# Optimization experiments

Hardware: AMD Instinct MI355X
Metric: run time of the kernel (lower is better)

## Reference

```python
import jax, jax.numpy as jnp
import numpy as np

B, IN, H, OUT, RANK = 2048, 256, 128, 128, 8
EPS = 1e-5

def setup_inputs() -> dict:
    key = jax.random.key(0)
    ks = jax.random.split(key, 9)
    inv = lambda n: 1.0 / np.sqrt(n)
    return {
        "X": jax.random.normal(ks[0], (B, IN), jnp.float32),
        "W1": jax.random.uniform(ks[1], (IN, H), jnp.float32, -inv(IN), inv(IN)),
        "b1": jnp.zeros((H,), jnp.float32),
        "W2": jax.random.uniform(ks[2], (IN, OUT), jnp.float32, -inv(IN), inv(IN)),
        "b2": jnp.zeros((OUT,), jnp.float32),
        "W3": jax.random.uniform(ks[3], (H, OUT), jnp.float32, -inv(H), inv(H)),
        "b3": jnp.zeros((OUT,), jnp.float32),
        "P": jax.random.normal(ks[4], (RANK, H, H, H), jnp.float32),  # (rank, p, q, k)
        "gz": jnp.ones((H,), jnp.float32),
        "bz": jnp.zeros((H,), jnp.float32),
        "gy": jnp.ones((H,), jnp.float32),
        "by": jnp.zeros((H,), jnp.float32),
    }

def _bn(x, g, b):
    # training-mode BatchNorm1d: batch stats, biased variance
    m = x.mean(axis=0)
    v = x.var(axis=0)
    return (x - m) * jax.lax.rsqrt(v + EPS) * g + b

def reference(X, W1, b1, W2, b2, W3, b3, P, gz, bz, gy, by):
    Z = jax.nn.relu(X @ W1 + b1)               # (B, H); dropout = identity (eval)

    def step(carry, Pi):
        Zi, Y = carry
        # batch_quadratic: out[b,k] = sum_{p,q} Zi[b,p] * Pi[p,q,k] * Z[b,q]
        Zi = jnp.einsum('bp,pqk,bq->bk', Zi, Pi, Z)
        Zi = _bn(Zi, gz, bz)
        return (Zi, Y + Zi / RANK), None

    Y0 = jnp.zeros((X.shape[0], H), X.dtype)
    (_, Y), _ = jax.lax.scan(step, (Z, Y0), P)
    Y = _bn(Y, gy, by)
    out = jax.nn.relu(jax.nn.relu(Y @ W3 + b3) + jax.nn.relu(X @ W2 + b2))
    return out
```

## Files before the change

### kernel.cpp

```cpp
#include <hip/hip_runtime.h>

typedef __bf16 bf16x8 __attribute__((ext_vector_type(8)));
typedef float  floatx4 __attribute__((ext_vector_type(4)));

constexpr int B_    = 2048;
constexpr int NIN   = 256;
constexpr int H_    = 128;
constexpr int RANK_ = 8;
constexpr float EPS_ = 1e-5f;

__global__ __launch_bounds__(256)
void k_head(const float* __restrict__ X,
            const float* __restrict__ W1, const float* __restrict__ b1,
            const float* __restrict__ W2, const float* __restrict__ b2,
            const float* __restrict__ P,
            float* __restrict__ Z, float* __restrict__ R2, __bf16* __restrict__ Zbf,
            __bf16* __restrict__ Pperm, float* __restrict__ stats ) {
    __shared__ float sT[32 * 129];
    const int bx = blockIdx.x, t = threadIdx.x;

    if (bx < RANK_ + 1) stats[bx * 256 + t] = 0.f;

    {
        const int row0 = bx * 2;
        sT[t]       = X[(size_t)row0       * NIN + t];
        sT[256 + t] = X[(size_t)(row0 + 1) * NIN + t];
        __syncthreads();
        const int col = t & 127, half = t >> 7;
        float s1 = 0.f, s2 = 0.f;
        const float* sxh = sT + half * 256;
#pragma unroll 8
        for (int i = 0; i < NIN; ++i) {
            s1 = fmaf(sxh[i], W1[i * H_ + col], s1);
            s2 = fmaf(sxh[i], W2[i * H_ + col], s2);
        }
        const int b = row0 + half;
        const float z = fmaxf(s1 + b1[col], 0.f);
        const float r = fmaxf(s2 + b2[col], 0.f);
        Z[(size_t)b * H_ + col]   = z;
        Zbf[(size_t)b * H_ + col] = (__bf16)z;
        R2[(size_t)b * H_ + col]  = r;
        __syncthreads();
    }
    {
        const int r = bx >> 7, p = bx & 127;
        const float4* Pp4 = (const float4*)(P + ((size_t)r * H_ + p) * (H_ * H_));
        __bf16* dst = Pperm + (size_t)r * (H_ * H_ * H_);
        const int L = t & 63, quad = L >> 4, lo = L & 15, g0 = t >> 6;
#pragma unroll
        for (int s = 0; s < 4; ++s) {
#pragma unroll
            for (int it = 0; it < 4; ++it) {
                const int idx = it * 256 + t;
                const int q = idx >> 5, k4 = idx & 31;
                const float4 v = Pp4[(size_t)(s * 32 + q) * 32 + k4];
                float* d = sT + q * 129 + k4 * 4;
                d[0] = v.x; d[1] = v.y; d[2] = v.z; d[3] = v.w;
            }
            __syncthreads();
#pragma unroll
            for (int gg = 0; gg < 2; ++gg) {
                const int g = g0 + 4 * gg;
                __bf16 v8[8];
#pragma unroll
                for (int j = 0; j < 8; ++j)
                    v8[j] = (__bf16)sT[(quad * 8 + j) * 129 + g * 16 + lo];
                *(bf16x8*)(dst + (((size_t)(g * 128 + p) * 4 + s) * 64 + L) * 8) =
                    *(const bf16x8*)v8;
            }
            __syncthreads();
        }
    }
}

__global__ __launch_bounds__(512, 2)
void k_rank(const __bf16* __restrict__ Pr, const __bf16* __restrict__ Zbf,
            const float* __restrict__ prevT, const float* __restrict__ prevStats,
            const float* __restrict__ gz, const float* __restrict__ bz,
            float* __restrict__ T, float* __restrict__ stats, const int first) {
    __shared__ float smem[8960];
    const int kg = blockIdx.x, mblk = blockIdx.y, b0 = mblk * 64;
    const int t = threadIdx.x;
    const int w = t >> 6, L = t & 63, quad = L >> 4, lo = L & 15;

    float* sAl = smem + 8704; float* sBe = smem + 8832;
    if (t < 128) {
        if (first) { sAl[t] = 1.f; sBe[t] = 0.f; }
        else {
            const float s1 = prevStats[t], s2 = prevStats[128 + t];
            const float mm = s1 * (1.f / B_);
            const float var = s2 * (1.f / B_) - mm * mm;
            const float a = rsqrtf(var + EPS_) * gz[t];
            sAl[t] = a; sBe[t] = bz[t] - mm * a;
        }
    }
    bf16x8 A[4][4];
#pragma unroll
    for (int mt = 0; mt < 4; ++mt)
#pragma unroll
        for (int ks = 0; ks < 4; ++ks)
            A[mt][ks] = *(const bf16x8*)(Zbf + (size_t)(b0 + mt * 16 + lo) * H_ + ks * 32 + quad * 8);
    __syncthreads();
    {
        const int sp = t & 127, rr = t >> 7;
        const float a = sAl[sp], be = sBe[sp];
#pragma unroll
        for (int i = 0; i < 16; ++i) {
            const int row = rr + 4 * i;
            smem[sp * 68 + row] = fmaf(prevT[(size_t)(b0 + row) * H_ + sp], a, be);
        }
    }
    __syncthreads();

    floatx4 acc[4];
#pragma unroll
    for (int mt = 0; mt < 4; ++mt) acc[mt] = (floatx4){0.f, 0.f, 0.f, 0.f};

    const bf16x8* Pb = (const bf16x8*)Pr;
    const int p0 = w * 16;
    const size_t fbase = ((size_t)kg * 128 + p0) * 4;
    bf16x8 Bf[4], Bn[4];
#pragma unroll
    for (int s = 0; s < 4; ++s) Bf[s] = Pb[(fbase + s) * 64 + L];

    for (int pp = 0; pp < 16; ++pp) {
        const int p = p0 + pp;
        if (pp < 15) {
#pragma unroll
            for (int s = 0; s < 4; ++s)
                Bn[s] = Pb[(fbase + (size_t)(pp + 1) * 4 + s) * 64 + L];
        }
        floatx4 S[4];
#pragma unroll
        for (int mt = 0; mt < 4; ++mt) S[mt] = (floatx4){0.f, 0.f, 0.f, 0.f};
#pragma unroll
        for (int ks = 0; ks < 4; ++ks)
#pragma unroll
            for (int mt = 0; mt < 4; ++mt)
                S[mt] = __builtin_amdgcn_mfma_f32_16x16x32_bf16(A[mt][ks], Bf[ks], S[mt], 0, 0, 0);
#pragma unroll
        for (int mt = 0; mt < 4; ++mt) {
            const floatx4 zi = *(const floatx4*)&smem[p * 68 + mt * 16 + quad * 4];
            acc[mt] += zi * S[mt];
        }
#pragma unroll
        for (int s = 0; s < 4; ++s) Bf[s] = Bn[s];
    }
    __syncthreads();
#pragma unroll
    for (int mt = 0; mt < 4; ++mt)
#pragma unroll
        for (int i = 0; i < 4; ++i)
            smem[w * 1024 + (mt * 4 + i) * 64 + L] = acc[mt][i];
    if (t < 32) smem[8192 + t] = 0.f;
    __syncthreads();

    float cs = 0.f, cs2 = 0.f;
#pragma unroll
    for (int k2 = 0; k2 < 2; ++k2) {
        const int e = t + 512 * k2;
        float v = 0.f;
#pragma unroll
        for (int q = 0; q < 8; ++q) v += smem[q * 1024 + e];
        const int j = e >> 6, L2 = e & 63;
        const int row = b0 + (j >> 2) * 16 + (L2 >> 4) * 4 + (j & 3);
        const int col = kg * 16 + (L2 & 15);
        T[(size_t)row * H_ + col] = v;
        cs += v; cs2 += v * v;
    }
    cs  += __shfl_xor(cs, 16);  cs  += __shfl_xor(cs, 32);
    cs2 += __shfl_xor(cs2, 16); cs2 += __shfl_xor(cs2, 32);
    if (L < 16) { atomicAdd(&smem[8192 + L], cs); atomicAdd(&smem[8208 + L], cs2); }
    __syncthreads();
    if (t < 16)      atomicAdd(&stats[kg * 16 + t],            smem[8192 + t]);
    else if (t < 32) atomicAdd(&stats[128 + kg * 16 + t - 16], smem[8192 + t]);
}

__global__ __launch_bounds__(256)
void k_y(const float* __restrict__ T, const float* __restrict__ sums,
         const float* __restrict__ gz, const float* __restrict__ bz,
         float* __restrict__ Y, float* __restrict__ ysums) {
    __shared__ float al[1024], be[1024], red[256];
    const int bx = blockIdx.x, t = threadIdx.x;
    for (int e = t; e < 1024; e += 256) {
        const int rr = e >> 7, k = e & 127;
        const float s1 = sums[rr * 256 + k], s2 = sums[rr * 256 + 128 + k];
        const float mm = s1 * (1.f / B_);
        const float var = s2 * (1.f / B_) - mm * mm;
        const float a = rsqrtf(var + EPS_) * gz[k];
        al[e] = a; be[e] = bz[k] - mm * a;
    }
    red[t] = 0.f;
    __syncthreads();
    const int col = t & 127, half = t >> 7;
    float ps = 0.f, ps2 = 0.f;
    for (int i = 0; i < 16; ++i) {
        const int b = bx * 32 + half + 2 * i;
        float y = 0.f;
#pragma unroll
        for (int rr = 0; rr < 8; ++rr)
            y += fmaf(T[(size_t)rr * B_ * H_ + (size_t)b * H_ + col],
                      al[rr * 128 + col], be[rr * 128 + col]);
        y *= (1.f / RANK_);
        Y[(size_t)b * H_ + col] = y;
        ps += y; ps2 += y * y;
    }
    atomicAdd(&red[col],       half == 0 ? ps  : 0.f);
    atomicAdd(&red[128 + col], half == 0 ? ps2 : 0.f);
    __syncthreads();
    atomicAdd(&red[col],       half == 1 ? ps  : 0.f);
    atomicAdd(&red[128 + col], half == 1 ? ps2 : 0.f);
    __syncthreads();
    if (t < 128) {
        atomicAdd(&ysums[t],       red[t]);
        atomicAdd(&ysums[128 + t], red[128 + t]);
    }
}

__global__ __launch_bounds__(256)
void k_out(const float* __restrict__ Y, const float* __restrict__ ystats,
           const float* __restrict__ gy, const float* __restrict__ by,
           const float* __restrict__ W3, const float* __restrict__ b3,
           const float* __restrict__ R2, float* __restrict__ out) {
    __shared__ float sy[8 * 132];
    const int bx = blockIdx.x, t = threadIdx.x;
    const int col = t & 127, rh = t >> 7;
    const int b0 = bx * 8;
    const float mm = ystats[col] * (1.f / B_);
    const float var = ystats[128 + col] * (1.f / B_) - mm * mm;
    const float ay = rsqrtf(var + EPS_) * gy[col];
    const float bb = by[col] - mm * ay;
#pragma unroll
    for (int i = 0; i < 4; ++i) {
        const int row = rh + 2 * i;
        sy[row * 132 + col] = fmaf(Y[(size_t)(b0 + row) * H_ + col], ay, bb);
    }
    __syncthreads();
#pragma unroll
    for (int j = 0; j < 4; ++j) {
        const int row = rh * 4 + j;
        float s = 0.f;
        const float* syr = sy + row * 132;
#pragma unroll 8
        for (int h = 0; h < H_; ++h)
            s = fmaf(syr[h], W3[h * H_ + col], s);
        const size_t gi = (size_t)(b0 + row) * H_ + col;
        out[gi] = fmaxf(fmaxf(s + b3[col], 0.f) + R2[gi], 0.f);
    }
}

extern "C" void kernel_launch(void* const* d_in, const int* in_sizes, int n_in,
                              void* d_out, int out_size, void* d_ws, size_t ws_size,
                              hipStream_t stream) {
    const float* X  = (const float*)d_in[0];
    const float* W1 = (const float*)d_in[1];
    const float* b1 = (const float*)d_in[2];
    const float* W2 = (const float*)d_in[3];
    const float* b2 = (const float*)d_in[4];
    const float* W3 = (const float*)d_in[5];
    const float* b3 = (const float*)d_in[6];
    const float* P  = (const float*)d_in[7];
    const float* gz = (const float*)d_in[8];
    const float* bz = (const float*)d_in[9];
    const float* gy = (const float*)d_in[10];
    const float* by = (const float*)d_in[11];
    float* out = (float*)d_out;

    const size_t rankElems = (size_t)H_ * H_ * H_;

    char* wsb = (char*)d_ws;
    float* Z      = (float*)wsb;   wsb += (size_t)B_ * H_ * 4;
    float* R2     = (float*)wsb;   wsb += (size_t)B_ * H_ * 4;
    float* Y      = (float*)wsb;   wsb += (size_t)B_ * H_ * 4;
    float* stats  = (float*)wsb;   wsb += (size_t)(RANK_ + 1) * 256 * 4;
    float* T      = (float*)wsb;   wsb += (size_t)RANK_ * B_ * H_ * 4;
    __bf16* Zbf   = (__bf16*)wsb;  wsb += (size_t)B_ * H_ * 2;
    __bf16* Pperm = (__bf16*)wsb;

    float* ysums = stats + RANK_ * 256;

    k_head<<<1024, 256, 0, stream>>>(X, W1, b1, W2, b2, P, Z, R2, Zbf, Pperm, stats);

    for (int r = 0; r < RANK_; ++r) {
        const float* prevT = (r == 0) ? Z : (T + (size_t)(r - 1) * B_ * H_);
        const float* prevS = (r == 0) ? stats : (stats + (r - 1) * 256);
        k_rank<<<dim3(8, 32), 512, 0, stream>>>(Pperm + (size_t)r * rankElems, Zbf,
                                                prevT, prevS, gz, bz,
                                                T + (size_t)r * B_ * H_, stats + r * 256,
                                                r == 0 ? 1 : 0);
    }

    k_y<<<64, 256, 0, stream>>>(T, stats, gz, bz, Y, ysums);
    k_out<<<256, 256, 0, stream>>>(Y, ysums, gy, by, W3, b3, R2, out);
}
```

Measured before the change: 303.1 us.

## Fuse Y accumulation into rank kernel and drop fp32 Z buffer

Each rank kernel's kg==0 blocks now accumulate the normalized previous-rank output into Y while staging it. k_y then only needs to add the final rank instead of rereading all eight T slices. The head kernel computes four rows per block, reusing W1/W2 loads, and no longer writes the fp32 Z, using the bf16 Z for rank 0 instead. This trades extra work in a subset of rank blocks and a slight precision change for less global memory traffic.

```diff
diff --git a/kernel.cpp b/kernel.cpp
--- a/kernel.cpp
+++ b/kernel.cpp
@@ -14,32 +14,37 @@
             const float* __restrict__ W1, const float* __restrict__ b1,
             const float* __restrict__ W2, const float* __restrict__ b2,
             const float* __restrict__ P,
-            float* __restrict__ Z, float* __restrict__ R2, __bf16* __restrict__ Zbf,
+            float* __restrict__ R2, __bf16* __restrict__ Zbf,
             __bf16* __restrict__ Pperm, float* __restrict__ stats ) {
-    __shared__ float sT[32 * 129];
+    __shared__ float smem[4160];
     const int bx = blockIdx.x, t = threadIdx.x;
 
     if (bx < RANK_ + 1) stats[bx * 256 + t] = 0.f;
 
-    {
-        const int row0 = bx * 2;
-        sT[t]       = X[(size_t)row0       * NIN + t];
-        sT[256 + t] = X[(size_t)(row0 + 1) * NIN + t];
+    if (bx < 512) {
+        const int b0 = bx * 4;
+#pragma unroll
+        for (int i = 0; i < 4; ++i) {
+            const int e = i * 256 + t;
+            smem[e] = X[(size_t)(b0 + (e >> 8)) * NIN + (e & 255)];
+        }
         __syncthreads();
-        const int col = t & 127, half = t >> 7;
-        float s1 = 0.f, s2 = 0.f;
-        const float* sxh = sT + half * 256;
+        const int col = t & 127, rh = t >> 7;
+        float s1a = 0.f, s2a = 0.f, s1b = 0.f, s2b = 0.f;
+        const float* sxa = smem + rh * 256;
+        const float* sxb = smem + (rh + 2) * 256;
 #pragma unroll 8
         for (int i = 0; i < NIN; ++i) {
-            s1 = fmaf(sxh[i], W1[i * H_ + col], s1);
-            s2 = fmaf(sxh[i], W2[i * H_ + col], s2);
-        }
-        const int b = row0 + half;
-        const float z = fmaxf(s1 + b1[col], 0.f);
-        const float r = fmaxf(s2 + b2[col], 0.f);
-        Z[(size_t)b * H_ + col]   = z;
-        Zbf[(size_t)b * H_ + col] = (__bf16)z;
-        R2[(size_t)b * H_ + col]  = r;
+            const float w1 = W1[i * H_ + col];
+            const float w2 = W2[i * H_ + col];
+            s1a = fmaf(sxa[i], w1, s1a);  s2a = fmaf(sxa[i], w2, s2a);
+            s1b = fmaf(sxb[i], w1, s1b);  s2b = fmaf(sxb[i], w2, s2b);
+        }
+        const int ba = b0 + rh, bb = b0 + rh + 2;
+        const float za = fmaxf(s1a + b1[col], 0.f), ra = fmaxf(s2a + b2[col], 0.f);
+        const float zb = fmaxf(s1b + b1[col], 0.f), rb = fmaxf(s2b + b2[col], 0.f);
+        Zbf[(size_t)ba * H_ + col] = (__bf16)za;  R2[(size_t)ba * H_ + col] = ra;
+        Zbf[(size_t)bb * H_ + col] = (__bf16)zb;  R2[(size_t)bb * H_ + col] = rb;
         __syncthreads();
     }
     {
@@ -54,7 +59,7 @@
                 const int idx = it * 256 + t;
                 const int q = idx >> 5, k4 = idx & 31;
                 const float4 v = Pp4[(size_t)(s * 32 + q) * 32 + k4];
-                float* d = sT + q * 129 + k4 * 4;
+                float* d = smem + q * 129 + k4 * 4;
                 d[0] = v.x; d[1] = v.y; d[2] = v.z; d[3] = v.w;
             }
             __syncthreads();
@@ -64,7 +69,7 @@
                 __bf16 v8[8];
 #pragma unroll
                 for (int j = 0; j < 8; ++j)
-                    v8[j] = (__bf16)sT[(quad * 8 + j) * 129 + g * 16 + lo];
+                    v8[j] = (__bf16)smem[(quad * 8 + j) * 129 + g * 16 + lo];
                 *(bf16x8*)(dst + (((size_t)(g * 128 + p) * 4 + s) * 64 + L) * 8) =
                     *(const bf16x8*)v8;
             }
@@ -77,22 +82,20 @@
 void k_rank(const __bf16* __restrict__ Pr, const __bf16* __restrict__ Zbf,
             const float* __restrict__ prevT, const float* __restrict__ prevStats,
             const float* __restrict__ gz, const float* __restrict__ bz,
-            float* __restrict__ T, float* __restrict__ stats, const int first) {
+            float* __restrict__ T, float* __restrict__ stats,
+            float* __restrict__ Y, const int ymode) {
     __shared__ float smem[8960];
     const int kg = blockIdx.x, mblk = blockIdx.y, b0 = mblk * 64;
     const int t = threadIdx.x;
     const int w = t >> 6, L = t & 63, quad = L >> 4, lo = L & 15;
 
     float* sAl = smem + 8704; float* sBe = smem + 8832;
-    if (t < 128) {
-        if (first) { sAl[t] = 1.f; sBe[t] = 0.f; }
-        else {
-            const float s1 = prevStats[t], s2 = prevStats[128 + t];
-            const float mm = s1 * (1.f / B_);
-            const float var = s2 * (1.f / B_) - mm * mm;
-            const float a = rsqrtf(var + EPS_) * gz[t];
-            sAl[t] = a; sBe[t] = bz[t] - mm * a;
-        }
+    if (ymode != 0 && t < 128) {
+        const float s1 = prevStats[t], s2 = prevStats[128 + t];
+        const float mm = s1 * (1.f / B_);
+        const float var = s2 * (1.f / B_) - mm * mm;
+        const float a = rsqrtf(var + EPS_) * gz[t];
+        sAl[t] = a; sBe[t] = bz[t] - mm * a;
     }
     bf16x8 A[4][4];
 #pragma unroll
@@ -100,21 +103,6 @@
 #pragma unroll
         for (int ks = 0; ks < 4; ++ks)
             A[mt][ks] = *(const bf16x8*)(Zbf + (size_t)(b0 + mt * 16 + lo) * H_ + ks * 32 + quad * 8);
-    __syncthreads();
-    {
-        const int sp = t & 127, rr = t >> 7;
-        const float a = sAl[sp], be = sBe[sp];
-#pragma unroll
-        for (int i = 0; i < 16; ++i) {
-            const int row = rr + 4 * i;
-            smem[sp * 68 + row] = fmaf(prevT[(size_t)(b0 + row) * H_ + sp], a, be);
-        }
-    }
-    __syncthreads();
-
-    floatx4 acc[4];
-#pragma unroll
-    for (int mt = 0; mt < 4; ++mt) acc[mt] = (floatx4){0.f, 0.f, 0.f, 0.f};
 
     const bf16x8* Pb = (const bf16x8*)Pr;
     const int p0 = w * 16;
@@ -122,6 +110,35 @@
     bf16x8 Bf[4], Bn[4];
 #pragma unroll
     for (int s = 0; s < 4; ++s) Bf[s] = Pb[(fbase + s) * 64 + L];
+
+    __syncthreads();
+    {
+        const int sp = t & 127, rr = t >> 7;
+        if (ymode == 0) {
+#pragma unroll
+            for (int i = 0; i < 16; ++i) {
+                const int row = rr + 4 * i;
+                smem[sp * 68 + row] = (float)Zbf[(size_t)(b0 + row) * H_ + sp];
+            }
+        } else {
+            const float a = sAl[sp], be = sBe[sp];
+#pragma unroll
+            for (int i = 0; i < 16; ++i) {
+                const int row = rr + 4 * i;
+                const float zin = fmaf(prevT[(size_t)(b0 + row) * H_ + sp], a, be);
+                smem[sp * 68 + row] = zin;
+                if (kg == 0) {
+                    float* yp = Y + (size_t)(b0 + row) * H_ + sp;
+                    *yp = (ymode == 1) ? zin * (1.f / RANK_) : fmaf(zin, 1.f / RANK_, *yp);
+                }
+            }
+        }
+    }
+    __syncthreads();
+
+    floatx4 acc[4];
+#pragma unroll
+    for (int mt = 0; mt < 4; ++mt) acc[mt] = (floatx4){0.f, 0.f, 0.f, 0.f};
 
     for (int pp = 0; pp < 16; ++pp) {
         const int p = p0 + pp;
@@ -177,32 +194,28 @@
 }
 
 __global__ __launch_bounds__(256)
-void k_y(const float* __restrict__ T, const float* __restrict__ sums,
+void k_y(const float* __restrict__ T7, const float* __restrict__ s7,
          const float* __restrict__ gz, const float* __restrict__ bz,
          float* __restrict__ Y, float* __restrict__ ysums) {
-    __shared__ float al[1024], be[1024], red[256];
+    __shared__ float sAl[128], sBe[128], red[256];
     const int bx = blockIdx.x, t = threadIdx.x;
-    for (int e = t; e < 1024; e += 256) {
-        const int rr = e >> 7, k = e & 127;
-        const float s1 = sums[rr * 256 + k], s2 = sums[rr * 256 + 128 + k];
+    if (t < 128) {
+        const float s1 = s7[t], s2 = s7[128 + t];
         const float mm = s1 * (1.f / B_);
         const float var = s2 * (1.f / B_) - mm * mm;
-        const float a = rsqrtf(var + EPS_) * gz[k];
-        al[e] = a; be[e] = bz[k] - mm * a;
+        const float a = rsqrtf(var + EPS_) * gz[t];
+        sAl[t] = a; sBe[t] = bz[t] - mm * a;
     }
     red[t] = 0.f;
     __syncthreads();
     const int col = t & 127, half = t >> 7;
+    const float a = sAl[col], be = sBe[col];
     float ps = 0.f, ps2 = 0.f;
     for (int i = 0; i < 16; ++i) {
         const int b = bx * 32 + half + 2 * i;
-        float y = 0.f;
-#pragma unroll
-        for (int rr = 0; rr < 8; ++rr)
-            y += fmaf(T[(size_t)rr * B_ * H_ + (size_t)b * H_ + col],
-                      al[rr * 128 + col], be[rr * 128 + col]);
-        y *= (1.f / RANK_);
-        Y[(size_t)b * H_ + col] = y;
+        const size_t gi = (size_t)b * H_ + col;
+        const float y = Y[gi] + fmaf(T7[gi], a, be) * (1.f / RANK_);
+        Y[gi] = y;
         ps += y; ps2 += y * y;
     }
     atomicAdd(&red[col],       half == 0 ? ps  : 0.f);
@@ -269,7 +282,6 @@
     const size_t rankElems = (size_t)H_ * H_ * H_;
 
     char* wsb = (char*)d_ws;
-    float* Z      = (float*)wsb;   wsb += (size_t)B_ * H_ * 4;
     float* R2     = (float*)wsb;   wsb += (size_t)B_ * H_ * 4;
     float* Y      = (float*)wsb;   wsb += (size_t)B_ * H_ * 4;
     float* stats  = (float*)wsb;   wsb += (size_t)(RANK_ + 1) * 256 * 4;
@@ -279,17 +291,18 @@
 
     float* ysums = stats + RANK_ * 256;
 
-    k_head<<<1024, 256, 0, stream>>>(X, W1, b1, W2, b2, P, Z, R2, Zbf, Pperm, stats);
+    k_head<<<1024, 256, 0, stream>>>(X, W1, b1, W2, b2, P, R2, Zbf, Pperm, stats);
 
     for (int r = 0; r < RANK_; ++r) {
-        const float* prevT = (r == 0) ? Z : (T + (size_t)(r - 1) * B_ * H_);
+        const float* prevT = (r == 0) ? (const float*)Zbf : (T + (size_t)(r - 1) * B_ * H_);
         const float* prevS = (r == 0) ? stats : (stats + (r - 1) * 256);
+        const int ymode = (r == 0) ? 0 : (r == 1 ? 1 : 2);
         k_rank<<<dim3(8, 32), 512, 0, stream>>>(Pperm + (size_t)r * rankElems, Zbf,
                                                 prevT, prevS, gz, bz,
                                                 T + (size_t)r * B_ * H_, stats + r * 256,
-                                                r == 0 ? 1 : 0);
-    }
-
-    k_y<<<64, 256, 0, stream>>>(T, stats, gz, bz, Y, ysums);
+                                                Y, ymode);
+    }
+
+    k_y<<<64, 256, 0, stream>>>(T + (size_t)7 * B_ * H_, stats + 7 * 256, gz, bz, Y, ysums);
     k_out<<<256, 256, 0, stream>>>(Y, ysums, gy, by, W3, b3, R2, out);
 }
```

After: 313.7 us. +3.5%, slower.
